# Optimization experiments

Measured on AMD Instinct MI355X. Metric: run time of the kernel, lower is better.

## Reference

```python
import jax, jax.numpy as jnp
import numpy as np

INPUT_DIM = 1024
HIDDEN_DIM = 1024


def setup_inputs() -> dict:
    key = jax.random.key(0)
    k1, k2, k3, k4, k5 = jax.random.split(key, 5)
    B, T = 64, 512
    bound_h = 1.0 / np.sqrt(HIDDEN_DIM)
    bound_x = 1.0 / np.sqrt(INPUT_DIM)
    return {
        "x_seq": jax.random.normal(k1, (B, T, INPUT_DIM), dtype=jnp.float32),
        "W_h": jax.random.uniform(k2, (HIDDEN_DIM, HIDDEN_DIM), jnp.float32, -bound_h, bound_h),
        "b_h": jax.random.uniform(k3, (HIDDEN_DIM,), jnp.float32, -bound_h, bound_h),
        "W_x": jax.random.uniform(k4, (HIDDEN_DIM, INPUT_DIM), jnp.float32, -bound_x, bound_x),
        "b_x": jax.random.uniform(k5, (HIDDEN_DIM,), jnp.float32, -bound_x, bound_x),
    }


def reference(x_seq, W_h, b_h, W_x, b_x):
    # Precompute input projection for all timesteps as one batched GEMM:
    # xp: [B, T, H]
    xp = jnp.einsum("bti,hi->bth", x_seq, W_x) + b_x
    B = x_seq.shape[0]
    h0 = jnp.zeros((B, HIDDEN_DIM), dtype=x_seq.dtype)

    def step(h, xp_t):
        # h: [B, H], xp_t: [B, H]
        h_new = jnp.tanh(h @ W_h.T + b_h + xp_t)
        return h_new, None

    # scan over time: xp transposed to [T, B, H]
    h_final, _ = jax.lax.scan(step, h0, jnp.swapaxes(xp, 0, 1))
    return h_final  # [B, H] — last hidden state per batch element
```

## Files before the change

### kernel.cpp

```cpp
#include <hip/hip_runtime.h>
#include <cmath>


#define Bsz 64
#define Tsz 512
#define Hsz 1024

typedef float  f32x4 __attribute__((ext_vector_type(4)));
typedef short  s16x8 __attribute__((ext_vector_type(8)));

__device__ __forceinline__ unsigned short f2bf(float f) {
  unsigned u = __float_as_uint(f);
  u += 0x7fff + ((u >> 16) & 1);
  return (unsigned short)(u >> 16);
}

__device__ __forceinline__ void pack8(unsigned short* d, float4 v0, float4 v1) {
  d[0] = f2bf(v0.x); d[1] = f2bf(v0.y); d[2] = f2bf(v0.z); d[3] = f2bf(v0.w);
  d[4] = f2bf(v1.x); d[5] = f2bf(v1.y); d[6] = f2bf(v1.z); d[7] = f2bf(v1.w);
}

__device__ __forceinline__ float fast_tanh(float x) {
  float e = __expf(2.0f * x);
  return 1.0f - 2.0f / (e + 1.0f);
}

__global__ __launch_bounds__(256) void xp_gemm_kernel(
    const float* __restrict__ x, const float* __restrict__ Wx,
    const float* __restrict__ bx, const float* __restrict__ bh,
    float* __restrict__ xp) {
  __shared__ unsigned short Al[64 * 32];
  __shared__ unsigned short Bl[64 * 32];

  const int tid  = threadIdx.x;
  const int w    = tid >> 6;
  const int lane = tid & 63;
  const int m    = lane & 15;
  const int q    = lane >> 4;
  const int row0 = blockIdx.x * 64;
  const int col0 = blockIdx.y * 64;

  f32x4 acc[4];
#pragma unroll
  for (int i = 0; i < 4; ++i) acc[i] = (f32x4){0.f, 0.f, 0.f, 0.f};

  const int sr = tid >> 2;
  const int sc = tid & 3;
  const int sw = sc ^ ((sr >> 1) & 3);

  for (int kt = 0; kt < 32; ++kt) {
    const int k0 = kt * 32 + sc * 8;
    {
      const float* p = x + (size_t)(row0 + sr) * 1024 + k0;
      pack8(&Al[sr * 32 + sw * 8], *(const float4*)p, *(const float4*)(p + 4));
    }
    {
      const float* p = Wx + (size_t)(col0 + sr) * 1024 + k0;
      pack8(&Bl[sr * 32 + sw * 8], *(const float4*)p, *(const float4*)(p + 4));
    }
    __syncthreads();
    const int arow = w * 16 + m;
    s16x8 a = *(const s16x8*)&Al[arow * 32 + ((q ^ ((arow >> 1) & 3)) << 3)];
#pragma unroll
    for (int nt = 0; nt < 4; ++nt) {
      const int nrow = nt * 16 + m;
      s16x8 b = *(const s16x8*)&Bl[nrow * 32 + ((q ^ ((nrow >> 1) & 3)) << 3)];
      acc[nt] = __builtin_amdgcn_mfma_f32_16x16x32_bf16(a, b, acc[nt], 0, 0, 0);
    }
    __syncthreads();
  }

#pragma unroll
  for (int nt = 0; nt < 4; ++nt) {
    const int col  = col0 + nt * 16 + m;
    const float bias = bx[col] + bh[col];
#pragma unroll
    for (int r = 0; r < 4; ++r) {
      const int rowg = row0 + w * 16 + q * 4 + r;
      const int b = rowg >> 9;
      const int t = rowg & 511;
      xp[(size_t)t * (Bsz * Hsz) + b * Hsz + col] = acc[nt][r] + bias;
    }
  }
}


__global__ __launch_bounds__(64, 1) void rnn_scan_kernel(
    const float* __restrict__ Wh, const float* __restrict__ xp,
    float* __restrict__ out,
    unsigned long long* __restrict__ ring, unsigned* __restrict__ flags) {
  __shared__ unsigned short Wl[16 * 1024];

  const int lane = threadIdx.x & 63;
  const int m    = lane & 15;
  const int q    = lane >> 4;
  const int gb   = blockIdx.x >> 6;
  const int gj   = blockIdx.x & 63;
  const int j0   = gj * 16;
  const int rb   = gb * 16;

  for (int i = 0; i < 32; ++i) {
    const int jr = i >> 1;
    const int c  = (i & 1) * 64 + lane;
    const float* p = Wh + (size_t)(j0 + jr) * 1024 + c * 8;
    pack8(&Wl[jr * 1024 + ((c ^ (jr & 7)) << 3)],
          *(const float4*)p, *(const float4*)(p + 4));
  }
  __syncthreads();

  unsigned* grpflags = flags + gb * 1024;
  unsigned* myflag   = grpflags + gj * 16;
  const unsigned* pollflag = grpflags + lane * 16;

  unsigned long long* const grp = ring + (size_t)gb * 4096;
  const int cons_off = q * 32 + m * 2;
  const int prod_off = (gj * 2 + (q >> 1)) * 32 + m * 2 + (q & 1);

  for (int t = 0; t < Tsz; ++t) {
    const float4 xv = *(const float4*)(
        xp + (size_t)t * (Bsz * Hsz) + (size_t)(rb + m) * Hsz + j0 + q * 4);
    const float* xf = (const float*)&xv;

    f32x4 acc0 = (f32x4){0.f, 0.f, 0.f, 0.f};
    f32x4 acc1 = (f32x4){0.f, 0.f, 0.f, 0.f};
    f32x4 acc2 = (f32x4){0.f, 0.f, 0.f, 0.f};
    f32x4 acc3 = (f32x4){0.f, 0.f, 0.f, 0.f};

    if (t > 0) {
      const unsigned tg = (unsigned)t;
      unsigned v = __hip_atomic_load(pollflag, __ATOMIC_RELAXED,
                                     __HIP_MEMORY_SCOPE_AGENT);
      while (!__all((int)(v >= tg))) {
        __builtin_amdgcn_s_sleep(1);
        v = __hip_atomic_load(pollflag, __ATOMIC_RELAXED,
                              __HIP_MEMORY_SCOPE_AGENT);
      }

      const unsigned long long* rbase =
          grp + (size_t)(t & 1) * 16384 + cons_off;
      unsigned long long d[64];
#pragma unroll
      for (int kk = 0; kk < 32; ++kk) {
        d[2 * kk]     = __hip_atomic_load(rbase + kk * 128,     __ATOMIC_RELAXED,
                                          __HIP_MEMORY_SCOPE_AGENT);
        d[2 * kk + 1] = __hip_atomic_load(rbase + kk * 128 + 1, __ATOMIC_RELAXED,
                                          __HIP_MEMORY_SCOPE_AGENT);
      }

#pragma unroll
      for (int kk = 0; kk < 32; ++kk) {
        union { unsigned long long u[2]; s16x8 v; } hb;
        hb.u[0] = d[2 * kk];
        hb.u[1] = d[2 * kk + 1];
        s16x8 wf = *(const s16x8*)&Wl[m * 1024 + (((kk * 4 + q) ^ (m & 7)) << 3)];
        f32x4& ac = ((kk & 3) == 0) ? acc0 : ((kk & 3) == 1) ? acc1
                   : ((kk & 3) == 2) ? acc2 : acc3;
        ac = __builtin_amdgcn_mfma_f32_16x16x32_bf16(wf, hb.v, ac, 0, 0, 0);
      }
    }

    const f32x4 accs = (acc0 + acc1) + (acc2 + acc3);
    float hv[4];
#pragma unroll
    for (int r = 0; r < 4; ++r) hv[r] = fast_tanh(accs[r] + xf[r]);

    if (t == Tsz - 1) {
      *(float4*)&out[(size_t)(rb + m) * Hsz + j0 + q * 4] =
          make_float4(hv[0], hv[1], hv[2], hv[3]);
    } else {
      const unsigned long long s =
          (unsigned long long)f2bf(hv[0])        |
          ((unsigned long long)f2bf(hv[1]) << 16) |
          ((unsigned long long)f2bf(hv[2]) << 32) |
          ((unsigned long long)f2bf(hv[3]) << 48);
      unsigned long long* wb =
          grp + (size_t)((t + 1) & 1) * 16384 + prod_off;
      __hip_atomic_store(wb, s, __ATOMIC_RELAXED, __HIP_MEMORY_SCOPE_AGENT);
      __asm__ __volatile__("s_waitcnt vmcnt(0)" ::: "memory");
      if (lane == 0)
        __hip_atomic_store(myflag, (unsigned)(t + 1), __ATOMIC_RELAXED,
                           __HIP_MEMORY_SCOPE_AGENT);
    }
  }
}

extern "C" void kernel_launch(void* const* d_in, const int* in_sizes, int n_in,
                              void* d_out, int out_size, void* d_ws, size_t ws_size,
                              hipStream_t stream) {
  (void)in_sizes; (void)n_in; (void)out_size; (void)ws_size;
  const float* x  = (const float*)d_in[0];
  const float* Wh = (const float*)d_in[1];
  const float* bh = (const float*)d_in[2];
  const float* Wx = (const float*)d_in[3];
  const float* bx = (const float*)d_in[4];
  float* out = (float*)d_out;

  char* ws = (char*)d_ws;
  unsigned*           flags = (unsigned*)ws;
  unsigned long long* ring  = (unsigned long long*)(ws + 65536);
  float*              xp    = (float*)(ws + (1 << 20));

  hipMemsetAsync(d_ws, 0, 16384, stream);

  dim3 g1(Bsz * Tsz / 64, Hsz / 64);
  xp_gemm_kernel<<<g1, dim3(256), 0, stream>>>(x, Wx, bx, bh, xp);
  rnn_scan_kernel<<<dim3(256), dim3(64), 0, stream>>>(Wh, xp, out, ring, flags);
}
```

Baseline: 1.761 ms.

## Hold W_h slices in registers, widen blocks to 32 columns, pipeline ring loads

The scan kernel now uses 128 workgroups, each owning 32 hidden columns, instead of 256 owning 16. This halves the number of producers each step must wait on and halves the flag polling. The bf16 W_h fragments now live entirely in VGPRs instead of LDS, which removes the LDS reads on the per-step critical path. Ring-buffer loads use inline-asm dwordx4 loads with cache-bypass bits, issued in four groups and staggered with waitcnt so the MFMAs overlap the remaining loads. The cost is very heavy register pressure (512 VGPRs' worth of weights) and spill risk.

```diff
diff --git a/kernel.cpp b/kernel.cpp
--- a/kernel.cpp
+++ b/kernel.cpp
@@ -85,46 +85,77 @@
 }
 
 
+#define HLOAD(D, g)                                                           \
+  do {                                                                        \
+    _Pragma("unroll")                                                         \
+    for (int f_ = 0; f_ < 8; ++f_) {                                          \
+      unsigned long long a_ = rb64 + (unsigned long long)(((g) * 8 + f_) * 1024); \
+      asm volatile("global_load_dwordx4 %0, %1, off sc0 sc1"                  \
+                   : "=v"(D[f_]) : "v"(a_) : "memory");                       \
+    }                                                                         \
+  } while (0)
+
+#define HMFMA(D, g)                                                           \
+  do {                                                                        \
+    _Pragma("unroll")                                                         \
+    for (int f_ = 0; f_ < 8; ++f_) {                                          \
+      const int kk_ = (g) * 8 + f_;                                           \
+      union { uint4 u; s16x8 v; } hb_; hb_.u = D[f_];                         \
+      if (kk_ & 1) {                                                          \
+        acc01 = __builtin_amdgcn_mfma_f32_16x16x32_bf16(wreg0[kk_], hb_.v, acc01, 0, 0, 0); \
+        acc11 = __builtin_amdgcn_mfma_f32_16x16x32_bf16(wreg1[kk_], hb_.v, acc11, 0, 0, 0); \
+      } else {                                                                \
+        acc00 = __builtin_amdgcn_mfma_f32_16x16x32_bf16(wreg0[kk_], hb_.v, acc00, 0, 0, 0); \
+        acc10 = __builtin_amdgcn_mfma_f32_16x16x32_bf16(wreg1[kk_], hb_.v, acc10, 0, 0, 0); \
+      }                                                                       \
+    }                                                                         \
+  } while (0)
+
 __global__ __launch_bounds__(64, 1) void rnn_scan_kernel(
     const float* __restrict__ Wh, const float* __restrict__ xp,
     float* __restrict__ out,
     unsigned long long* __restrict__ ring, unsigned* __restrict__ flags) {
-  __shared__ unsigned short Wl[16 * 1024];
-
   const int lane = threadIdx.x & 63;
   const int m    = lane & 15;
   const int q    = lane >> 4;
-  const int gb   = blockIdx.x >> 6;
-  const int gj   = blockIdx.x & 63;
-  const int j0   = gj * 16;
+  const int gb   = blockIdx.x >> 5;
+  const int jb   = blockIdx.x & 31;
+  const int j0   = jb * 32;
   const int rb   = gb * 16;
 
-  for (int i = 0; i < 32; ++i) {
-    const int jr = i >> 1;
-    const int c  = (i & 1) * 64 + lane;
-    const float* p = Wh + (size_t)(j0 + jr) * 1024 + c * 8;
-    pack8(&Wl[jr * 1024 + ((c ^ (jr & 7)) << 3)],
-          *(const float4*)p, *(const float4*)(p + 4));
-  }
-  __syncthreads();
-
-  unsigned* grpflags = flags + gb * 1024;
-  unsigned* myflag   = grpflags + gj * 16;
-  const unsigned* pollflag = grpflags + lane * 16;
+  s16x8 wreg0[32], wreg1[32];
+#pragma unroll
+  for (int kk = 0; kk < 32; ++kk) {
+    const float* p0 = Wh + (size_t)(j0 + m) * 1024 + kk * 32 + q * 8;
+    const float* p1 = Wh + (size_t)(j0 + 16 + m) * 1024 + kk * 32 + q * 8;
+    float4 a0 = *(const float4*)p0, b0 = *(const float4*)(p0 + 4);
+    float4 a1 = *(const float4*)p1, b1 = *(const float4*)(p1 + 4);
+    s16x8 w0, w1;
+    w0[0]=f2bf(a0.x); w0[1]=f2bf(a0.y); w0[2]=f2bf(a0.z); w0[3]=f2bf(a0.w);
+    w0[4]=f2bf(b0.x); w0[5]=f2bf(b0.y); w0[6]=f2bf(b0.z); w0[7]=f2bf(b0.w);
+    w1[0]=f2bf(a1.x); w1[1]=f2bf(a1.y); w1[2]=f2bf(a1.z); w1[3]=f2bf(a1.w);
+    w1[4]=f2bf(b1.x); w1[5]=f2bf(b1.y); w1[6]=f2bf(b1.z); w1[7]=f2bf(b1.w);
+    wreg0[kk] = w0; wreg1[kk] = w1;
+  }
+
+  unsigned* myflag = flags + (gb * 32 + jb) * 16;
+  const unsigned* pollflag = flags + (gb * 32 + (lane & 31)) * 16;
 
   unsigned long long* const grp = ring + (size_t)gb * 4096;
-  const int cons_off = q * 32 + m * 2;
-  const int prod_off = (gj * 2 + (q >> 1)) * 32 + m * 2 + (q & 1);
+  const int prod0 = (jb * 4 + 0 + (q >> 1)) * 32 + m * 2 + (q & 1);
+  const int prod1 = (jb * 4 + 2 + (q >> 1)) * 32 + m * 2 + (q & 1);
+  const int cons_byte = q * 256 + m * 16;
 
   for (int t = 0; t < Tsz; ++t) {
-    const float4 xv = *(const float4*)(
-        xp + (size_t)t * (Bsz * Hsz) + (size_t)(rb + m) * Hsz + j0 + q * 4);
-    const float* xf = (const float*)&xv;
-
-    f32x4 acc0 = (f32x4){0.f, 0.f, 0.f, 0.f};
-    f32x4 acc1 = (f32x4){0.f, 0.f, 0.f, 0.f};
-    f32x4 acc2 = (f32x4){0.f, 0.f, 0.f, 0.f};
-    f32x4 acc3 = (f32x4){0.f, 0.f, 0.f, 0.f};
+    const float* xpt =
+        xp + (size_t)t * (Bsz * Hsz) + (size_t)(rb + m) * Hsz + j0 + q * 4;
+    const float4 xv0 = *(const float4*)xpt;
+    const float4 xv1 = *(const float4*)(xpt + 16);
+
+    f32x4 acc00 = (f32x4){0.f, 0.f, 0.f, 0.f};
+    f32x4 acc01 = (f32x4){0.f, 0.f, 0.f, 0.f};
+    f32x4 acc10 = (f32x4){0.f, 0.f, 0.f, 0.f};
+    f32x4 acc11 = (f32x4){0.f, 0.f, 0.f, 0.f};
 
     if (t > 0) {
       const unsigned tg = (unsigned)t;
@@ -135,48 +166,59 @@
         v = __hip_atomic_load(pollflag, __ATOMIC_RELAXED,
                               __HIP_MEMORY_SCOPE_AGENT);
       }
-
-      const unsigned long long* rbase =
-          grp + (size_t)(t & 1) * 16384 + cons_off;
-      unsigned long long d[64];
-#pragma unroll
-      for (int kk = 0; kk < 32; ++kk) {
-        d[2 * kk]     = __hip_atomic_load(rbase + kk * 128,     __ATOMIC_RELAXED,
-                                          __HIP_MEMORY_SCOPE_AGENT);
-        d[2 * kk + 1] = __hip_atomic_load(rbase + kk * 128 + 1, __ATOMIC_RELAXED,
-                                          __HIP_MEMORY_SCOPE_AGENT);
-      }
-
-#pragma unroll
-      for (int kk = 0; kk < 32; ++kk) {
-        union { unsigned long long u[2]; s16x8 v; } hb;
-        hb.u[0] = d[2 * kk];
-        hb.u[1] = d[2 * kk + 1];
-        s16x8 wf = *(const s16x8*)&Wl[m * 1024 + (((kk * 4 + q) ^ (m & 7)) << 3)];
-        f32x4& ac = ((kk & 3) == 0) ? acc0 : ((kk & 3) == 1) ? acc1
-                   : ((kk & 3) == 2) ? acc2 : acc3;
-        ac = __builtin_amdgcn_mfma_f32_16x16x32_bf16(wf, hb.v, ac, 0, 0, 0);
-      }
-    }
-
-    const f32x4 accs = (acc0 + acc1) + (acc2 + acc3);
-    float hv[4];
-#pragma unroll
-    for (int r = 0; r < 4; ++r) hv[r] = fast_tanh(accs[r] + xf[r]);
+      const unsigned long long rb64 =
+          (unsigned long long)(const char*)(grp + (size_t)(t & 1) * 16384) +
+          (unsigned)cons_byte;
+
+      uint4 hA[8], hB[8], hC[8], hD[8];
+      HLOAD(hA, 0); HLOAD(hB, 1); HLOAD(hC, 2); HLOAD(hD, 3);
+      asm volatile("s_waitcnt vmcnt(24)" ::: "memory");
+      __builtin_amdgcn_sched_barrier(0);
+      HMFMA(hA, 0);
+      asm volatile("s_waitcnt vmcnt(16)" ::: "memory");
+      __builtin_amdgcn_sched_barrier(0);
+      HMFMA(hB, 1);
+      asm volatile("s_waitcnt vmcnt(8)" ::: "memory");
+      __builtin_amdgcn_sched_barrier(0);
+      HMFMA(hC, 2);
+      asm volatile("s_waitcnt vmcnt(0)" ::: "memory");
+      __builtin_amdgcn_sched_barrier(0);
+      HMFMA(hD, 3);
+    }
+
+    const f32x4 a0 = acc00 + acc01;
+    const f32x4 a1 = acc10 + acc11;
+    const float* xf0 = (const float*)&xv0;
+    const float* xf1 = (const float*)&xv1;
+    float hv0[4], hv1[4];
+#pragma unroll
+    for (int r = 0; r < 4; ++r) {
+      hv0[r] = fast_tanh(a0[r] + xf0[r]);
+      hv1[r] = fast_tanh(a1[r] + xf1[r]);
+    }
 
     if (t == Tsz - 1) {
       *(float4*)&out[(size_t)(rb + m) * Hsz + j0 + q * 4] =
-          make_float4(hv[0], hv[1], hv[2], hv[3]);
+          make_float4(hv0[0], hv0[1], hv0[2], hv0[3]);
+      *(float4*)&out[(size_t)(rb + m) * Hsz + j0 + 16 + q * 4] =
+          make_float4(hv1[0], hv1[1], hv1[2], hv1[3]);
     } else {
-      const unsigned long long s =
-          (unsigned long long)f2bf(hv[0])        |
-          ((unsigned long long)f2bf(hv[1]) << 16) |
-          ((unsigned long long)f2bf(hv[2]) << 32) |
-          ((unsigned long long)f2bf(hv[3]) << 48);
-      unsigned long long* wb =
-          grp + (size_t)((t + 1) & 1) * 16384 + prod_off;
-      __hip_atomic_store(wb, s, __ATOMIC_RELAXED, __HIP_MEMORY_SCOPE_AGENT);
-      __asm__ __volatile__("s_waitcnt vmcnt(0)" ::: "memory");
+      const unsigned long long s0 =
+          (unsigned long long)f2bf(hv0[0])        |
+          ((unsigned long long)f2bf(hv0[1]) << 16) |
+          ((unsigned long long)f2bf(hv0[2]) << 32) |
+          ((unsigned long long)f2bf(hv0[3]) << 48);
+      const unsigned long long s1 =
+          (unsigned long long)f2bf(hv1[0])        |
+          ((unsigned long long)f2bf(hv1[1]) << 16) |
+          ((unsigned long long)f2bf(hv1[2]) << 32) |
+          ((unsigned long long)f2bf(hv1[3]) << 48);
+      unsigned long long* wb = grp + (size_t)((t + 1) & 1) * 16384;
+      __hip_atomic_store(wb + prod0, s0, __ATOMIC_RELAXED,
+                         __HIP_MEMORY_SCOPE_AGENT);
+      __hip_atomic_store(wb + prod1, s1, __ATOMIC_RELAXED,
+                         __HIP_MEMORY_SCOPE_AGENT);
+      asm volatile("s_waitcnt vmcnt(0)" ::: "memory");
       if (lane == 0)
         __hip_atomic_store(myflag, (unsigned)(t + 1), __ATOMIC_RELAXED,
                            __HIP_MEMORY_SCOPE_AGENT);
@@ -204,5 +246,5 @@
 
   dim3 g1(Bsz * Tsz / 64, Hsz / 64);
   xp_gemm_kernel<<<g1, dim3(256), 0, stream>>>(x, Wx, bx, bh, xp);
-  rnn_scan_kernel<<<dim3(256), dim3(64), 0, stream>>>(Wh, xp, out, ring, flags);
-}
+  rnn_scan_kernel<<<dim3(128), dim3(64), 0, stream>>>(Wh, xp, out, ring, flags);
+}
```

New measurement: 1.952 ms. 10.8% more time.

## Merge four scan waves per block, keep W_h in registers, share h via LDS

Applied to the files above, without the earlier changes.

The recurrent scan kernel now runs 64 blocks of four waves instead of 256 single-wave blocks. Each wave keeps its bf16 slice of W_h in registers rather than LDS. The block loads the previous hidden state from the global ring cooperatively into a double-buffered LDS tile, so each block does one global read instead of four. Each batch group now has 16 flags to poll instead of 64, which cuts cross-block synchronisation traffic, but each step adds two block barriers and more register pressure.

```diff
diff --git a/kernel.cpp b/kernel.cpp
--- a/kernel.cpp
+++ b/kernel.cpp
@@ -85,41 +85,46 @@
 }
 
 
-__global__ __launch_bounds__(64, 1) void rnn_scan_kernel(
+__global__ __launch_bounds__(256, 1) void rnn_scan_kernel(
     const float* __restrict__ Wh, const float* __restrict__ xp,
     float* __restrict__ out,
     unsigned long long* __restrict__ ring, unsigned* __restrict__ flags) {
-  __shared__ unsigned short Wl[16 * 1024];
-
-  const int lane = threadIdx.x & 63;
+  __shared__ unsigned long long Hl[2][4096];
+
+  const int tid  = threadIdx.x;
+  const int w    = tid >> 6;
+  const int lane = tid & 63;
   const int m    = lane & 15;
   const int q    = lane >> 4;
-  const int gb   = blockIdx.x >> 6;
-  const int gj   = blockIdx.x & 63;
-  const int j0   = gj * 16;
+  const int gb   = blockIdx.x >> 4;
+  const int jb   = blockIdx.x & 15;
+  const int j0   = jb * 64 + w * 16;
   const int rb   = gb * 16;
 
-  for (int i = 0; i < 32; ++i) {
-    const int jr = i >> 1;
-    const int c  = (i & 1) * 64 + lane;
-    const float* p = Wh + (size_t)(j0 + jr) * 1024 + c * 8;
-    pack8(&Wl[jr * 1024 + ((c ^ (jr & 7)) << 3)],
-          *(const float4*)p, *(const float4*)(p + 4));
-  }
-  __syncthreads();
-
-  unsigned* grpflags = flags + gb * 1024;
-  unsigned* myflag   = grpflags + gj * 16;
-  const unsigned* pollflag = grpflags + lane * 16;
+  s16x8 wreg[32];
+#pragma unroll
+  for (int kk = 0; kk < 32; ++kk) {
+    const float* p = Wh + (size_t)(j0 + m) * 1024 + kk * 32 + q * 8;
+    float4 a = *(const float4*)p, b = *(const float4*)(p + 4);
+    s16x8 wv;
+    wv[0]=f2bf(a.x); wv[1]=f2bf(a.y); wv[2]=f2bf(a.z); wv[3]=f2bf(a.w);
+    wv[4]=f2bf(b.x); wv[5]=f2bf(b.y); wv[6]=f2bf(b.z); wv[7]=f2bf(b.w);
+    wreg[kk] = wv;
+  }
+
+  unsigned* myflag = flags + gb * 16 + jb;
+  const unsigned* pollflag = flags + gb * 16 + (lane & 15);
 
   unsigned long long* const grp = ring + (size_t)gb * 4096;
-  const int cons_off = q * 32 + m * 2;
+  const int gj    = jb * 4 + w;
   const int prod_off = (gj * 2 + (q >> 1)) * 32 + m * 2 + (q & 1);
+  const int cons_u64 = q * 32 + m * 2;
 
   for (int t = 0; t < Tsz; ++t) {
     const float4 xv = *(const float4*)(
         xp + (size_t)t * (Bsz * Hsz) + (size_t)(rb + m) * Hsz + j0 + q * 4);
     const float* xf = (const float*)&xv;
+    const int p = t & 1;
 
     f32x4 acc0 = (f32x4){0.f, 0.f, 0.f, 0.f};
     f32x4 acc1 = (f32x4){0.f, 0.f, 0.f, 0.f};
@@ -136,26 +141,24 @@
                               __HIP_MEMORY_SCOPE_AGENT);
       }
 
-      const unsigned long long* rbase =
-          grp + (size_t)(t & 1) * 16384 + cons_off;
-      unsigned long long d[64];
+      const unsigned long long* src =
+          grp + (size_t)p * 16384 + w * 1024 + lane;
+      unsigned long long d[16];
+#pragma unroll
+      for (int i = 0; i < 16; ++i)
+        d[i] = __hip_atomic_load(src + i * 64, __ATOMIC_RELAXED,
+                                 __HIP_MEMORY_SCOPE_AGENT);
+#pragma unroll
+      for (int i = 0; i < 16; ++i)
+        Hl[p][w * 1024 + i * 64 + lane] = d[i];
+      __syncthreads();
+
 #pragma unroll
       for (int kk = 0; kk < 32; ++kk) {
-        d[2 * kk]     = __hip_atomic_load(rbase + kk * 128,     __ATOMIC_RELAXED,
-                                          __HIP_MEMORY_SCOPE_AGENT);
-        d[2 * kk + 1] = __hip_atomic_load(rbase + kk * 128 + 1, __ATOMIC_RELAXED,
-                                          __HIP_MEMORY_SCOPE_AGENT);
-      }
-
-#pragma unroll
-      for (int kk = 0; kk < 32; ++kk) {
-        union { unsigned long long u[2]; s16x8 v; } hb;
-        hb.u[0] = d[2 * kk];
-        hb.u[1] = d[2 * kk + 1];
-        s16x8 wf = *(const s16x8*)&Wl[m * 1024 + (((kk * 4 + q) ^ (m & 7)) << 3)];
+        const s16x8 hb = *(const s16x8*)&Hl[p][kk * 128 + cons_u64];
         f32x4& ac = ((kk & 3) == 0) ? acc0 : ((kk & 3) == 1) ? acc1
                    : ((kk & 3) == 2) ? acc2 : acc3;
-        ac = __builtin_amdgcn_mfma_f32_16x16x32_bf16(wf, hb.v, ac, 0, 0, 0);
+        ac = __builtin_amdgcn_mfma_f32_16x16x32_bf16(wreg[kk], hb, ac, 0, 0, 0);
       }
     }
 
@@ -173,11 +176,12 @@
           ((unsigned long long)f2bf(hv[1]) << 16) |
           ((unsigned long long)f2bf(hv[2]) << 32) |
           ((unsigned long long)f2bf(hv[3]) << 48);
-      unsigned long long* wb =
-          grp + (size_t)((t + 1) & 1) * 16384 + prod_off;
-      __hip_atomic_store(wb, s, __ATOMIC_RELAXED, __HIP_MEMORY_SCOPE_AGENT);
-      __asm__ __volatile__("s_waitcnt vmcnt(0)" ::: "memory");
-      if (lane == 0)
+      unsigned long long* wb = grp + (size_t)((t + 1) & 1) * 16384;
+      __hip_atomic_store(wb + prod_off, s, __ATOMIC_RELAXED,
+                         __HIP_MEMORY_SCOPE_AGENT);
+      asm volatile("s_waitcnt vmcnt(0)" ::: "memory");
+      __syncthreads();
+      if (tid == 0)
         __hip_atomic_store(myflag, (unsigned)(t + 1), __ATOMIC_RELAXED,
                            __HIP_MEMORY_SCOPE_AGENT);
     }
@@ -204,5 +208,5 @@
 
   dim3 g1(Bsz * Tsz / 64, Hsz / 64);
   xp_gemm_kernel<<<g1, dim3(256), 0, stream>>>(x, Wx, bx, bh, xp);
-  rnn_scan_kernel<<<dim3(256), dim3(64), 0, stream>>>(Wh, xp, out, ring, flags);
-}
+  rnn_scan_kernel<<<dim3(64), dim3(256), 0, stream>>>(Wh, xp, out, ring, flags);
+}
```

Result: slower. 2.139 ms (+21.4%).

## Fuse input-projection GEMM and recurrent scan into one persistent kernel

Applied to the files above, without the earlier changes.

Merges the xp GEMM and the RNN scan into a single launch. The first 64 blocks run the scan, each packing four batch groups as four waves. The remaining blocks compute xp tiles ordered by time chunk and signal per-chunk completion counters, which the scan polls before consuming each 64-step chunk. This lets the serial scan start while the GEMM for later timesteps is still running, hiding GEMM time behind the latency-bound recurrence. Risks include contention between GEMM blocks and scan blocks on the same CUs, deadlock if scan blocks are not resident, and scan waves raising their priority.

```diff
diff --git a/kernel.cpp b/kernel.cpp
--- a/kernel.cpp
+++ b/kernel.cpp
@@ -25,88 +25,98 @@
   return 1.0f - 2.0f / (e + 1.0f);
 }
 
-__global__ __launch_bounds__(256) void xp_gemm_kernel(
-    const float* __restrict__ x, const float* __restrict__ Wx,
-    const float* __restrict__ bx, const float* __restrict__ bh,
-    float* __restrict__ xp) {
+
+__global__ __launch_bounds__(256, 1) void fused_kernel(
+    const float* __restrict__ x,  const float* __restrict__ Wh,
+    const float* __restrict__ bh, const float* __restrict__ Wx,
+    const float* __restrict__ bx,
+    float* __restrict__ xp, float* __restrict__ out,
+    unsigned long long* __restrict__ ring, unsigned* __restrict__ flags,
+    unsigned* __restrict__ cnt) {
   __shared__ unsigned short Al[64 * 32];
   __shared__ unsigned short Bl[64 * 32];
+  __shared__ unsigned short Wl[16 * 1024];
 
   const int tid  = threadIdx.x;
   const int w    = tid >> 6;
   const int lane = tid & 63;
   const int m    = lane & 15;
   const int q    = lane >> 4;
-  const int row0 = blockIdx.x * 64;
-  const int col0 = blockIdx.y * 64;
-
-  f32x4 acc[4];
-#pragma unroll
-  for (int i = 0; i < 4; ++i) acc[i] = (f32x4){0.f, 0.f, 0.f, 0.f};
-
-  const int sr = tid >> 2;
-  const int sc = tid & 3;
-  const int sw = sc ^ ((sr >> 1) & 3);
-
-  for (int kt = 0; kt < 32; ++kt) {
-    const int k0 = kt * 32 + sc * 8;
-    {
-      const float* p = x + (size_t)(row0 + sr) * 1024 + k0;
-      pack8(&Al[sr * 32 + sw * 8], *(const float4*)p, *(const float4*)(p + 4));
-    }
-    {
-      const float* p = Wx + (size_t)(col0 + sr) * 1024 + k0;
-      pack8(&Bl[sr * 32 + sw * 8], *(const float4*)p, *(const float4*)(p + 4));
-    }
+
+  if (blockIdx.x >= 64) {
+    const int g   = blockIdx.x - 64;
+    const int c   = g >> 10;
+    const int b   = (g >> 4) & 63;
+    const int ct  = g & 15;
+    const int row0 = b * 512 + c * 64;
+    const int col0 = ct * 64;
+
+    f32x4 acc[4];
+#pragma unroll
+    for (int i = 0; i < 4; ++i) acc[i] = (f32x4){0.f, 0.f, 0.f, 0.f};
+
+    const int sr = tid >> 2;
+    const int sc = tid & 3;
+    const int sw = sc ^ ((sr >> 1) & 3);
+
+    for (int kt = 0; kt < 32; ++kt) {
+      const int k0 = kt * 32 + sc * 8;
+      {
+        const float* p = x + (size_t)(row0 + sr) * 1024 + k0;
+        pack8(&Al[sr * 32 + sw * 8], *(const float4*)p, *(const float4*)(p + 4));
+      }
+      {
+        const float* p = Wx + (size_t)(col0 + sr) * 1024 + k0;
+        pack8(&Bl[sr * 32 + sw * 8], *(const float4*)p, *(const float4*)(p + 4));
+      }
+      __syncthreads();
+      const int arow = w * 16 + m;
+      s16x8 a = *(const s16x8*)&Al[arow * 32 + ((q ^ ((arow >> 1) & 3)) << 3)];
+#pragma unroll
+      for (int nt = 0; nt < 4; ++nt) {
+        const int nrow = nt * 16 + m;
+        s16x8 bb = *(const s16x8*)&Bl[nrow * 32 + ((q ^ ((nrow >> 1) & 3)) << 3)];
+        acc[nt] = __builtin_amdgcn_mfma_f32_16x16x32_bf16(a, bb, acc[nt], 0, 0, 0);
+      }
+      __syncthreads();
+    }
+
+#pragma unroll
+    for (int nt = 0; nt < 4; ++nt) {
+      const int col  = col0 + nt * 16 + m;
+      const float bias = bx[col] + bh[col];
+#pragma unroll
+      for (int r = 0; r < 4; ++r) {
+        const int rowg = row0 + w * 16 + q * 4 + r;
+        const int bb = rowg >> 9;
+        const int tt = rowg & 511;
+        unsigned* px = (unsigned*)&xp[(size_t)tt * (Bsz * Hsz) + bb * Hsz + col];
+        __hip_atomic_store(px, __float_as_uint(acc[nt][r] + bias),
+                           __ATOMIC_RELAXED, __HIP_MEMORY_SCOPE_AGENT);
+      }
+    }
+    asm volatile("s_waitcnt vmcnt(0)" ::: "memory");
     __syncthreads();
-    const int arow = w * 16 + m;
-    s16x8 a = *(const s16x8*)&Al[arow * 32 + ((q ^ ((arow >> 1) & 3)) << 3)];
-#pragma unroll
-    for (int nt = 0; nt < 4; ++nt) {
-      const int nrow = nt * 16 + m;
-      s16x8 b = *(const s16x8*)&Bl[nrow * 32 + ((q ^ ((nrow >> 1) & 3)) << 3)];
-      acc[nt] = __builtin_amdgcn_mfma_f32_16x16x32_bf16(a, b, acc[nt], 0, 0, 0);
-    }
-    __syncthreads();
+    if (tid == 0)
+      __hip_atomic_fetch_add(&cnt[c], 1u, __ATOMIC_RELAXED,
+                             __HIP_MEMORY_SCOPE_AGENT);
+    return;
   }
 
-#pragma unroll
-  for (int nt = 0; nt < 4; ++nt) {
-    const int col  = col0 + nt * 16 + m;
-    const float bias = bx[col] + bh[col];
-#pragma unroll
-    for (int r = 0; r < 4; ++r) {
-      const int rowg = row0 + w * 16 + q * 4 + r;
-      const int b = rowg >> 9;
-      const int t = rowg & 511;
-      xp[(size_t)t * (Bsz * Hsz) + b * Hsz + col] = acc[nt][r] + bias;
-    }
-  }
-}
-
-
-__global__ __launch_bounds__(64, 1) void rnn_scan_kernel(
-    const float* __restrict__ Wh, const float* __restrict__ xp,
-    float* __restrict__ out,
-    unsigned long long* __restrict__ ring, unsigned* __restrict__ flags) {
-  __shared__ unsigned short Wl[16 * 1024];
-
-  const int lane = threadIdx.x & 63;
-  const int m    = lane & 15;
-  const int q    = lane >> 4;
-  const int gb   = blockIdx.x >> 6;
-  const int gj   = blockIdx.x & 63;
-  const int j0   = gj * 16;
-  const int rb   = gb * 16;
-
-  for (int i = 0; i < 32; ++i) {
-    const int jr = i >> 1;
-    const int c  = (i & 1) * 64 + lane;
-    const float* p = Wh + (size_t)(j0 + jr) * 1024 + c * 8;
-    pack8(&Wl[jr * 1024 + ((c ^ (jr & 7)) << 3)],
+  const int gb = w;
+  const int gj = blockIdx.x;
+  const int j0 = gj * 16;
+  const int rb = gb * 16;
+
+  for (int i = 0; i < 8; ++i) {
+    const int jr  = i * 2 + (tid >> 7);
+    const int cch = tid & 127;
+    const float* p = Wh + (size_t)(j0 + jr) * 1024 + cch * 8;
+    pack8(&Wl[jr * 1024 + ((cch ^ (jr & 7)) << 3)],
           *(const float4*)p, *(const float4*)(p + 4));
   }
   __syncthreads();
+  __builtin_amdgcn_s_setprio(1);
 
   unsigned* grpflags = flags + gb * 1024;
   unsigned* myflag   = grpflags + gj * 16;
@@ -115,8 +125,20 @@
   unsigned long long* const grp = ring + (size_t)gb * 4096;
   const int cons_off = q * 32 + m * 2;
   const int prod_off = (gj * 2 + (q >> 1)) * 32 + m * 2 + (q & 1);
+  const int jl = m;
 
   for (int t = 0; t < Tsz; ++t) {
+    if ((t & 63) == 0) {
+      const unsigned ci = (unsigned)(t >> 6);
+      unsigned cv = __hip_atomic_load(&cnt[ci], __ATOMIC_RELAXED,
+                                      __HIP_MEMORY_SCOPE_AGENT);
+      while (cv < 1024u) {
+        __builtin_amdgcn_s_sleep(8);
+        cv = __hip_atomic_load(&cnt[ci], __ATOMIC_RELAXED,
+                               __HIP_MEMORY_SCOPE_AGENT);
+      }
+    }
+
     const float4 xv = *(const float4*)(
         xp + (size_t)t * (Bsz * Hsz) + (size_t)(rb + m) * Hsz + j0 + q * 4);
     const float* xf = (const float*)&xv;
@@ -152,7 +174,7 @@
         union { unsigned long long u[2]; s16x8 v; } hb;
         hb.u[0] = d[2 * kk];
         hb.u[1] = d[2 * kk + 1];
-        s16x8 wf = *(const s16x8*)&Wl[m * 1024 + (((kk * 4 + q) ^ (m & 7)) << 3)];
+        s16x8 wf = *(const s16x8*)&Wl[jl * 1024 + (((kk * 4 + q) ^ (jl & 7)) << 3)];
         f32x4& ac = ((kk & 3) == 0) ? acc0 : ((kk & 3) == 1) ? acc1
                    : ((kk & 3) == 2) ? acc2 : acc3;
         ac = __builtin_amdgcn_mfma_f32_16x16x32_bf16(wf, hb.v, ac, 0, 0, 0);
@@ -173,10 +195,10 @@
           ((unsigned long long)f2bf(hv[1]) << 16) |
           ((unsigned long long)f2bf(hv[2]) << 32) |
           ((unsigned long long)f2bf(hv[3]) << 48);
-      unsigned long long* wb =
-          grp + (size_t)((t + 1) & 1) * 16384 + prod_off;
-      __hip_atomic_store(wb, s, __ATOMIC_RELAXED, __HIP_MEMORY_SCOPE_AGENT);
-      __asm__ __volatile__("s_waitcnt vmcnt(0)" ::: "memory");
+      unsigned long long* wb = grp + (size_t)((t + 1) & 1) * 16384;
+      __hip_atomic_store(wb + prod_off, s, __ATOMIC_RELAXED,
+                         __HIP_MEMORY_SCOPE_AGENT);
+      asm volatile("s_waitcnt vmcnt(0)" ::: "memory");
       if (lane == 0)
         __hip_atomic_store(myflag, (unsigned)(t + 1), __ATOMIC_RELAXED,
                            __HIP_MEMORY_SCOPE_AGENT);
@@ -197,12 +219,12 @@
 
   char* ws = (char*)d_ws;
   unsigned*           flags = (unsigned*)ws;
+  unsigned*           cnt   = (unsigned*)(ws + 16384);
   unsigned long long* ring  = (unsigned long long*)(ws + 65536);
   float*              xp    = (float*)(ws + (1 << 20));
 
-  hipMemsetAsync(d_ws, 0, 16384, stream);
-
-  dim3 g1(Bsz * Tsz / 64, Hsz / 64);
-  xp_gemm_kernel<<<g1, dim3(256), 0, stream>>>(x, Wx, bx, bh, xp);
-  rnn_scan_kernel<<<dim3(256), dim3(64), 0, stream>>>(Wh, xp, out, ring, flags);
-}
+  hipMemsetAsync(d_ws, 0, 32768, stream);
+
+  fused_kernel<<<dim3(64 + 8192), dim3(256), 0, stream>>>(
+      x, Wh, bh, Wx, bx, xp, out, ring, flags, cnt);
+}
```

Result: slower. 2.606 ms (+48.0%).
